# Kernel optimization log

Hardware: AMD Instinct MI355X
Metric: run time of the kernel (lower is better)

Reference implementation:

```python
import jax, jax.numpy as jnp
import numpy as np

B, S, D = 1, 2048, 2048
N_HEAD, N_KV = 32, 8
HD = D // N_HEAD  # 64


def make_freqs_cis(seq_len, head_dim, base=10000.0):
    inv = 1.0 / (base ** (np.arange(0, head_dim, 2, dtype=np.float32) / head_dim))
    t = np.arange(seq_len, dtype=np.float32)
    f = np.outer(t, inv)  # [S, HD/2]
    return jnp.asarray(np.stack([np.cos(f), np.sin(f)], axis=-1))  # [S, HD/2, 2]


def setup_inputs() -> dict:
    key = jax.random.key(0)
    k1, k2, k3 = jax.random.split(key, 3)
    scale = 1.0 / np.sqrt(D)
    return {
        "hidden_states": jax.random.normal(k1, (B, S, D), jnp.float32),
        "freqs_cis": make_freqs_cis(S, HD),
        "wqkv": jax.random.normal(k2, ((N_HEAD + 2 * N_KV) * HD, D), jnp.float32) * scale,
        "wo": jax.random.normal(k3, (D, D), jnp.float32) * scale,
    }


def apply_rotary(x, freqs_cis):
    # x: [B, S, H, HD]; freqs_cis: [S, HD/2, 2]
    xs = x.reshape(*x.shape[:-1], HD // 2, 2)
    cos = freqs_cis[None, :, None, :, 0]
    sin = freqs_cis[None, :, None, :, 1]
    x0, x1 = xs[..., 0], xs[..., 1]
    out = jnp.stack([x0 * cos - x1 * sin, x1 * cos + x0 * sin], axis=-1)
    return out.reshape(x.shape)


def reference(hidden_states, freqs_cis, wqkv, wo):
    bsz, seq_len, _ = hidden_states.shape
    kv_size = N_KV * HD
    qkv = hidden_states @ wqkv.T  # [B, S, 3072]
    q, k, v = jnp.split(qkv, [D, D + kv_size], axis=-1)
    q = q.reshape(bsz, seq_len, N_HEAD, HD)
    k = k.reshape(bsz, seq_len, N_KV, HD)
    v = v.reshape(bsz, seq_len, N_KV, HD)
    q = apply_rotary(q, freqs_cis)
    k = apply_rotary(k, freqs_cis)
    # [B, H, S, HD]
    q = q.transpose(0, 2, 1, 3)
    k = k.transpose(0, 2, 1, 3)
    v = v.transpose(0, 2, 1, 3)
    rep = N_HEAD // N_KV
    k = jnp.repeat(k, rep, axis=1)
    v = jnp.repeat(v, rep, axis=1)
    scores = jnp.einsum("bhqd,bhkd->bhqk", q, k) / jnp.sqrt(jnp.float32(HD))
    causal = jnp.tril(jnp.ones((seq_len, seq_len), bool))
    scores = jnp.where(causal[None, None], scores, jnp.finfo(scores.dtype).min)
    attn = jax.nn.softmax(scores, axis=-1)
    out = jnp.einsum("bhqk,bhkd->bhqd", attn, v)
    out = out.transpose(0, 2, 1, 3).reshape(bsz, seq_len, D)
    return out @ wo.T
```

## Files before the change

### kernel.cpp

```cpp
#include <hip/hip_runtime.h>

typedef unsigned short u16;
typedef __attribute__((ext_vector_type(8))) short bf16x8;
typedef __attribute__((ext_vector_type(4))) float f32x4;

#define MFMA16(a, b, c) __builtin_amdgcn_mfma_f32_16x16x32_bf16((a), (b), (c), 0, 0, 0)
#define EXP2(x) __builtin_amdgcn_exp2f(x)

#define S 2048
#define D 2048
#define NH 32
#define NKV 8
#define HD 64
#define QKV_N 3072

__device__ __forceinline__ u16 f2bf(float f) {
  unsigned int u = __float_as_uint(f);
  u += 0x7fffu + ((u >> 16) & 1u);
  return (u16)(u >> 16);
}

__device__ __forceinline__ void glds16(const void* g, void* l) {
  __builtin_amdgcn_global_load_lds((const __attribute__((address_space(1))) unsigned int*)g,
                                   (__attribute__((address_space(3))) unsigned int*)l,
                                   16, 0, 0);
}

#define N1 (S * D / 4)
#define N2 (QKV_N * D / 4)
#define N3 (D * D / 4)
__global__ void cast_all(const float* __restrict__ hs, const float* __restrict__ wqkv,
                         const float* __restrict__ wo, u16* __restrict__ o1,
                         u16* __restrict__ o2, u16* __restrict__ o3) {
  int i = blockIdx.x * blockDim.x + threadIdx.x;
  const float* src;
  u16* dst;
  int idx;
  if (i < N1) { src = hs; dst = o1; idx = i; }
  else if (i < N1 + N2) { src = wqkv; dst = o2; idx = i - N1; }
  else if (i < N1 + N2 + N3) { src = wo; dst = o3; idx = i - N1 - N2; }
  else return;
  float4 v = ((const float4*)src)[idx];
  ushort4 o;
  o.x = f2bf(v.x); o.y = f2bf(v.y); o.z = f2bf(v.z); o.w = f2bf(v.w);
  ((ushort4*)dst)[idx] = o;
}

#define GEMM_MAINLOOP(A_, B_, K_, bm_, bn_)                                            \
  const int srowS = lane >> 3, scolS = ((lane & 7) ^ srowS) * 8;                       \
  const int aBase = wave * 32, bBase = wave * 16;                                      \
  const int qq = lane >> 4, sw = lr & 7;                                               \
  _Pragma("unroll") for (int c2 = 0; c2 < 4; ++c2)                                     \
      glds16(A_ + (size_t)(bm_ + aBase + c2 * 8 + srowS) * K_ + scolS,                 \
             &sA[0][aBase + c2 * 8][0]);                                               \
  _Pragma("unroll") for (int c2 = 0; c2 < 2; ++c2)                                     \
      glds16(B_ + (size_t)(bn_ + bBase + c2 * 8 + srowS) * K_ + scolS,                 \
             &sB[0][bBase + c2 * 8][0]);                                               \
  const int nk = K_ >> 6;                                                              \
  for (int it = 0; it < nk; ++it) {                                                    \
    const int buf = it & 1;                                                            \
    __syncthreads();                                                                   \
    if (it + 1 < nk) {                                                                 \
      const int k1 = (it + 1) << 6;                                                    \
      _Pragma("unroll") for (int c2 = 0; c2 < 4; ++c2)                                 \
          glds16(A_ + (size_t)(bm_ + aBase + c2 * 8 + srowS) * K_ + k1 + scolS,        \
                 &sA[buf ^ 1][aBase + c2 * 8][0]);                                     \
      _Pragma("unroll") for (int c2 = 0; c2 < 2; ++c2)                                 \
          glds16(B_ + (size_t)(bn_ + bBase + c2 * 8 + srowS) * K_ + k1 + scolS,        \
                 &sB[buf ^ 1][bBase + c2 * 8][0]);                                     \
    }                                                                                  \
    bf16x8 af[2][2], bfr[2][4];                                                        \
    _Pragma("unroll") for (int c = 0; c < 2; ++c) {                                    \
      const int pc = (((c << 2) | qq) ^ sw) * 8;     \
      _Pragma("unroll") for (int i = 0; i < 2; ++i)                                    \
          af[c][i] = *(const bf16x8*)(&sA[buf][wr + i * 16 + lr][pc]);                 \
      _Pragma("unroll") for (int j = 0; j < 4; ++j)                                    \
          bfr[c][j] = *(const bf16x8*)(&sB[buf][j * 16 + lr][pc]);                     \
    }                                                                                  \
    _Pragma("unroll") for (int c = 0; c < 2; ++c)                                      \
        _Pragma("unroll") for (int i = 0; i < 2; ++i)                                  \
            _Pragma("unroll") for (int j = 0; j < 4; ++j)                              \
                acc[i][j] = MFMA16(af[c][i], bfr[c][j], acc[i][j]);                    \
  }

__global__ __launch_bounds__(256) void gemm_bt(const u16* __restrict__ A, const u16* __restrict__ B,
                                               float* __restrict__ C, int M, int N, int K) {
  __shared__ u16 sA[2][128][64];
  __shared__ u16 sB[2][64][64];
  const int tid = threadIdx.x;
  const int wave = tid >> 6, lane = tid & 63;
  const int bm = blockIdx.y * 128, bn = blockIdx.x * 64;
  const int lr = lane & 15, lk = (lane >> 4) * 8;
  const int wr = wave * 32;
  (void)lk;

  f32x4 acc[2][4] = {};
  GEMM_MAINLOOP(A, B, K, bm, bn)

  const int crb = (lane >> 4) * 4;
#pragma unroll
  for (int i = 0; i < 2; ++i)
#pragma unroll
    for (int j = 0; j < 4; ++j)
#pragma unroll
      for (int r = 0; r < 4; ++r) {
        int row = bm + wr + i * 16 + crb + r;
        int col = bn + j * 16 + lr;
        C[(size_t)row * N + col] = acc[i][j][r];
      }
}

#define QSCALE 0.18033688011112042f
__global__ __launch_bounds__(256) void gemm1_fused(const u16* __restrict__ A, const u16* __restrict__ B,
                                                   const float* __restrict__ fc,
                                                   u16* __restrict__ qo, u16* __restrict__ ko,
                                                   u16* __restrict__ vt) {
  __shared__ u16 sA[2][128][64];
  __shared__ u16 sB[2][64][64];
  const int tid = threadIdx.x;
  const int wave = tid >> 6, lane = tid & 63;
  const int bm = blockIdx.y * 128, bn = blockIdx.x * 64;
  const int lr = lane & 15, lk = (lane >> 4) * 8;
  const int wr = wave * 32;
  (void)lk;

  f32x4 acc[2][4] = {};
  GEMM_MAINLOOP(A, B, D, bm, bn)

  const int crb = (lane >> 4) * 4;

  if (bn < 2560) {
    const bool isQ = (bn < 2048);
    u16* dst_base = isQ ? (qo + (size_t)(bn >> 6) * S * HD)
                        : (ko + (size_t)((bn - 2048) >> 6) * S * HD);
    const float scale = isQ ? QSCALE : 1.0f;
    const int odd = lr & 1;
#pragma unroll
    for (int i = 0; i < 2; ++i)
#pragma unroll
      for (int r = 0; r < 4; ++r) {
        const int srow = bm + wr + i * 16 + crb + r;
#pragma unroll
        for (int j = 0; j < 4; ++j) {
          const int d = j * 16 + lr;
          float x = acc[i][j][r];
          float xp = __shfl_xor(x, 1, 64);
          float2 cs = *(const float2*)(fc + (size_t)srow * 64 + (d >> 1) * 2);
          float y = odd ? (x * cs.x + xp * cs.y) : (x * cs.x - xp * cs.y);
          dst_base[(size_t)srow * HD + d] = f2bf(y * scale);
        }
      }
  } else {
    const int kvh = (bn - 2560) >> 6;
    __syncthreads();
    u16(*sT)[136] = (u16(*)[136]) & sA[0][0][0];
#pragma unroll
    for (int i = 0; i < 2; ++i)
#pragma unroll
      for (int j = 0; j < 4; ++j)
#pragma unroll
        for (int r = 0; r < 4; ++r)
          sT[j * 16 + lr][wr + i * 16 + crb + r] = f2bf(acc[i][j][r]);
    __syncthreads();
    const int d = tid >> 2, sc = (tid & 3) * 32;
    uint4* dst = (uint4*)(vt + (size_t)kvh * HD * S + (size_t)d * S + bm + sc);
    const uint4* src = (const uint4*)(&sT[d][sc]);
    dst[0] = src[0];
    dst[1] = src[1];
    dst[2] = src[2];
    dst[3] = src[3];
  }
}

__global__ __launch_bounds__(256, 2) void attn_kernel(const u16* __restrict__ Q, const u16* __restrict__ Kc,
                                                      const u16* __restrict__ Vt, u16* __restrict__ Out) {
  __shared__ u16 sK[64][72];
  __shared__ u16 sV[64][72];
  __shared__ u16 sP[4][2][16][72];

  const int p = blockIdx.x;
  const int h = blockIdx.y;
  const int kvh = h >> 2;
  const int tid = threadIdx.x;
  const int wave = tid >> 6, lane = tid & 63;
  const int lr = lane & 15;
  const int lk = (lane >> 4) * 8;
  const int crb = (lane >> 4) * 4;
  const int t = 4 * p + wave;
  const int qbA = 16 * t;
  const int qbB = 16 * (127 - t);

  const u16* qpA = Q + ((size_t)h * S + qbA + lr) * HD;
  const u16* qpB = Q + ((size_t)h * S + qbB + lr) * HD;
  bf16x8 aA0 = *(const bf16x8*)(qpA + lk);
  bf16x8 aA1 = *(const bf16x8*)(qpA + 32 + lk);
  bf16x8 aB0 = *(const bf16x8*)(qpB + lk);
  bf16x8 aB1 = *(const bf16x8*)(qpB + 32 + lk);

  const u16* Kh = Kc + (size_t)kvh * S * HD;
  const u16* Vh = Vt + (size_t)kvh * HD * S;

  const int sr0 = tid >> 3, so0 = (tid & 7) * 8;
  const int sr1 = sr0 + 32;

  float lA[4] = {0.f, 0.f, 0.f, 0.f}, lB[4] = {0.f, 0.f, 0.f, 0.f};
  f32x4 oA[4] = {}, oB[4] = {};

  const int kend = (32 - p) * 64;

  uint4 pk0 = *(const uint4*)(Kh + (size_t)sr0 * HD + so0);
  uint4 pk1 = *(const uint4*)(Kh + (size_t)sr1 * HD + so0);
  uint4 pv0 = *(const uint4*)(Vh + (size_t)sr0 * S + so0);
  uint4 pv1 = *(const uint4*)(Vh + (size_t)sr1 * S + so0);

  bf16x8 vf[4][2];
  bf16x8 pfB[2], pfA[2];
  bool prevA = false;

  for (int kb = 0; kb < kend; kb += 64) {
    if (kb > 0) {
#pragma unroll
      for (int tt = 0; tt < 4; ++tt) {
        oB[tt] = MFMA16(pfB[0], vf[tt][0], oB[tt]);
        oB[tt] = MFMA16(pfB[1], vf[tt][1], oB[tt]);
      }
      if (prevA) {
#pragma unroll
        for (int tt = 0; tt < 4; ++tt) {
          oA[tt] = MFMA16(pfA[0], vf[tt][0], oA[tt]);
          oA[tt] = MFMA16(pfA[1], vf[tt][1], oA[tt]);
        }
      }
    }

    *(uint4*)(&sK[sr0][so0]) = pk0;
    *(uint4*)(&sK[sr1][so0]) = pk1;
    *(uint4*)(&sV[sr0][so0]) = pv0;
    *(uint4*)(&sV[sr1][so0]) = pv1;
    __syncthreads();

    const int kn = kb + 64;
    if (kn < kend) {
      pk0 = *(const uint4*)(Kh + (size_t)(kn + sr0) * HD + so0);
      pk1 = *(const uint4*)(Kh + (size_t)(kn + sr1) * HD + so0);
      pv0 = *(const uint4*)(Vh + (size_t)sr0 * S + kn + so0);
      pv1 = *(const uint4*)(Vh + (size_t)sr1 * S + kn + so0);
    }

    const bool liveA = (kb <= qbA + 15);

    f32x4 cA[4], cB[4];
#pragma unroll
    for (int tt = 0; tt < 4; ++tt) {
      bf16x8 b0 = *(const bf16x8*)(&sK[tt * 16 + lr][lk]);
      bf16x8 b1 = *(const bf16x8*)(&sK[tt * 16 + lr][32 + lk]);
      f32x4 zB = {};
      zB = MFMA16(aB0, b0, zB);
      cB[tt] = MFMA16(aB1, b1, zB);
      if (liveA) {
        f32x4 zA = {};
        zA = MFMA16(aA0, b0, zA);
        cA[tt] = MFMA16(aA1, b1, zA);
      }
    }

    if (kb + 63 <= qbB) {
#pragma unroll
      for (int r = 0; r < 4; ++r)
#pragma unroll
        for (int tt = 0; tt < 4; ++tt) {
          float pp = EXP2(cB[tt][r] - 8.0f);
          lB[r] += pp;
          sP[wave][0][crb + r][tt * 16 + lr] = f2bf(pp);
        }
    } else {
#pragma unroll
      for (int r = 0; r < 4; ++r) {
        const int qr = qbB + crb + r;
#pragma unroll
        for (int tt = 0; tt < 4; ++tt) {
          float pp = (kb + tt * 16 + lr <= qr) ? EXP2(cB[tt][r] - 8.0f) : 0.0f;
          lB[r] += pp;
          sP[wave][0][crb + r][tt * 16 + lr] = f2bf(pp);
        }
      }
    }

    if (liveA) {
      if (kb + 63 <= qbA) {
#pragma unroll
        for (int r = 0; r < 4; ++r)
#pragma unroll
          for (int tt = 0; tt < 4; ++tt) {
            float pp = EXP2(cA[tt][r] - 8.0f);
            lA[r] += pp;
            sP[wave][1][crb + r][tt * 16 + lr] = f2bf(pp);
          }
      } else {
#pragma unroll
        for (int r = 0; r < 4; ++r) {
          const int qr = qbA + crb + r;
#pragma unroll
          for (int tt = 0; tt < 4; ++tt) {
            float pp = (kb + tt * 16 + lr <= qr) ? EXP2(cA[tt][r] - 8.0f) : 0.0f;
            lA[r] += pp;
            sP[wave][1][crb + r][tt * 16 + lr] = f2bf(pp);
          }
        }
      }
    }

    pfB[0] = *(const bf16x8*)(&sP[wave][0][lr][lk]);
    pfB[1] = *(const bf16x8*)(&sP[wave][0][lr][32 + lk]);
    if (liveA) {
      pfA[0] = *(const bf16x8*)(&sP[wave][1][lr][lk]);
      pfA[1] = *(const bf16x8*)(&sP[wave][1][lr][32 + lk]);
    }
#pragma unroll
    for (int tt = 0; tt < 4; ++tt) {
      vf[tt][0] = *(const bf16x8*)(&sV[tt * 16 + lr][lk]);
      vf[tt][1] = *(const bf16x8*)(&sV[tt * 16 + lr][32 + lk]);
    }
    prevA = liveA;
    __syncthreads();
  }

#pragma unroll
  for (int tt = 0; tt < 4; ++tt) {
    oB[tt] = MFMA16(pfB[0], vf[tt][0], oB[tt]);
    oB[tt] = MFMA16(pfB[1], vf[tt][1], oB[tt]);
  }
  if (prevA) {
#pragma unroll
    for (int tt = 0; tt < 4; ++tt) {
      oA[tt] = MFMA16(pfA[0], vf[tt][0], oA[tt]);
      oA[tt] = MFMA16(pfA[1], vf[tt][1], oA[tt]);
    }
  }

#pragma unroll
  for (int r = 0; r < 4; ++r) {
#pragma unroll
    for (int off = 1; off < 16; off <<= 1) {
      lA[r] += __shfl_xor(lA[r], off, 64);
      lB[r] += __shfl_xor(lB[r], off, 64);
    }
    lA[r] = 1.0f / lA[r];
    lB[r] = 1.0f / lB[r];
  }
#pragma unroll
  for (int tt = 0; tt < 4; ++tt)
#pragma unroll
    for (int r = 0; r < 4; ++r) {
      const int d = tt * 16 + lr;
      Out[(size_t)(qbA + crb + r) * D + h * HD + d] = f2bf(oA[tt][r] * lA[r]);
      Out[(size_t)(qbB + crb + r) * D + h * HD + d] = f2bf(oB[tt][r] * lB[r]);
    }
}

extern "C" void kernel_launch(void* const* d_in, const int* in_sizes, int n_in,
                              void* d_out, int out_size, void* d_ws, size_t ws_size,
                              hipStream_t stream) {
  const float* hs = (const float*)d_in[0];
  const float* fc = (const float*)d_in[1];
  const float* wqkv = (const float*)d_in[2];
  const float* wo = (const float*)d_in[3];
  float* out = (float*)d_out;
  char* ws = (char*)d_ws;

  u16* hs_bf   = (u16*)(ws);
  u16* wqkv_bf = (u16*)(ws + ((size_t)8 << 20));
  u16* wo_bf   = (u16*)(ws + ((size_t)20 << 20));
  u16* q_bf    = (u16*)(ws + ((size_t)28 << 20));
  u16* k_bf    = (u16*)(ws + ((size_t)36 << 20));
  u16* vt_bf   = (u16*)(ws + ((size_t)38 << 20));
  u16* attn_bf = (u16*)(ws + ((size_t)40 << 20));

  cast_all<<<(N1 + N2 + N3 + 255) / 256, 256, 0, stream>>>(hs, wqkv, wo, hs_bf, wqkv_bf, wo_bf);

  gemm1_fused<<<dim3(QKV_N / 64, S / 128), 256, 0, stream>>>(hs_bf, wqkv_bf, fc, q_bf, k_bf, vt_bf);

  attn_kernel<<<dim3(16, NH), 256, 0, stream>>>(q_bf, k_bf, vt_bf, attn_bf);

  gemm_bt<<<dim3(D / 64, S / 128), 256, 0, stream>>>(attn_bf, wo_bf, out, S, D, D);
}
```

Measured before the change: 204.6 us.

## Keep attention probabilities in registers via transposed QK and permlane packing

Swaps the QK^T MFMA operand order so each lane holds the score rows in the layout the PV MFMA needs as its A operand. Probabilities are then packed to bf16 with v_cvt_pk_bf16_f32 and redistributed with permlane32/16 swaps, so the per-wave LDS buffer and its store/load round trip go away. The row-sum bookkeeping becomes one scalar per lane, reduced at the end with cross-group shuffles. The risk is the exact lane mapping of the permlane shuffles, which must be right for the output to be correct.

```diff
diff --git a/kernel.cpp b/kernel.cpp
--- a/kernel.cpp
+++ b/kernel.cpp
@@ -24,6 +24,29 @@
   __builtin_amdgcn_global_load_lds((const __attribute__((address_space(1))) unsigned int*)g,
                                    (__attribute__((address_space(3))) unsigned int*)l,
                                    16, 0, 0);
+}
+
+__device__ __forceinline__ unsigned int cvtpk(float lo, float hi) {
+  unsigned int r;
+  asm("v_cvt_pk_bf16_f32 %0, %1, %2" : "=v"(r) : "v"(lo), "v"(hi));
+  return r;
+}
+__device__ __forceinline__ void swap32(unsigned int& a, unsigned int& b) {
+  asm("v_permlane32_swap_b32 %0, %1" : "+v"(a), "+v"(b));
+}
+__device__ __forceinline__ void swap16(unsigned int& a, unsigned int& b) {
+  asm("v_permlane16_swap_b32 %0, %1" : "+v"(a), "+v"(b));
+}
+__device__ __forceinline__ bf16x8 pack4(const f32x4 c0, const f32x4 c1) {
+  unsigned int x0 = cvtpk(c0[0], c0[1]);
+  unsigned int x1 = cvtpk(c0[2], c0[3]);
+  unsigned int y0 = cvtpk(c1[0], c1[1]);
+  unsigned int y1 = cvtpk(c1[2], c1[3]);
+  swap32(x0, y0); swap16(x0, y0);
+  swap32(x1, y1); swap16(x1, y1);
+  union { bf16x8 v; unsigned int u[4]; } r;
+  r.u[0] = x0; r.u[1] = x1; r.u[2] = y0; r.u[3] = y1;
+  return r.v;
 }
 
 #define N1 (S * D / 4)
@@ -176,7 +199,6 @@
                                                       const u16* __restrict__ Vt, u16* __restrict__ Out) {
   __shared__ u16 sK[64][72];
   __shared__ u16 sV[64][72];
-  __shared__ u16 sP[4][2][16][72];
 
   const int p = blockIdx.x;
   const int h = blockIdx.y;
@@ -203,7 +225,7 @@
   const int sr0 = tid >> 3, so0 = (tid & 7) * 8;
   const int sr1 = sr0 + 32;
 
-  float lA[4] = {0.f, 0.f, 0.f, 0.f}, lB[4] = {0.f, 0.f, 0.f, 0.f};
+  float lA = 0.f, lB = 0.f;
   f32x4 oA[4] = {}, oB[4] = {};
 
   const int kend = (32 - p) * 64;
@@ -255,72 +277,74 @@
       bf16x8 b0 = *(const bf16x8*)(&sK[tt * 16 + lr][lk]);
       bf16x8 b1 = *(const bf16x8*)(&sK[tt * 16 + lr][32 + lk]);
       f32x4 zB = {};
-      zB = MFMA16(aB0, b0, zB);
-      cB[tt] = MFMA16(aB1, b1, zB);
+      zB = MFMA16(b0, aB0, zB);
+      cB[tt] = MFMA16(b1, aB1, zB);
       if (liveA) {
         f32x4 zA = {};
-        zA = MFMA16(aA0, b0, zA);
-        cA[tt] = MFMA16(aA1, b1, zA);
-      }
-    }
-
-    if (kb + 63 <= qbB) {
-#pragma unroll
-      for (int r = 0; r < 4; ++r)
-#pragma unroll
-        for (int tt = 0; tt < 4; ++tt) {
-          float pp = EXP2(cB[tt][r] - 8.0f);
-          lB[r] += pp;
-          sP[wave][0][crb + r][tt * 16 + lr] = f2bf(pp);
-        }
-    } else {
-#pragma unroll
-      for (int r = 0; r < 4; ++r) {
-        const int qr = qbB + crb + r;
-#pragma unroll
-        for (int tt = 0; tt < 4; ++tt) {
-          float pp = (kb + tt * 16 + lr <= qr) ? EXP2(cB[tt][r] - 8.0f) : 0.0f;
-          lB[r] += pp;
-          sP[wave][0][crb + r][tt * 16 + lr] = f2bf(pp);
-        }
-      }
-    }
-
-    if (liveA) {
-      if (kb + 63 <= qbA) {
-#pragma unroll
-        for (int r = 0; r < 4; ++r)
-#pragma unroll
-          for (int tt = 0; tt < 4; ++tt) {
-            float pp = EXP2(cA[tt][r] - 8.0f);
-            lA[r] += pp;
-            sP[wave][1][crb + r][tt * 16 + lr] = f2bf(pp);
-          }
-      } else {
-#pragma unroll
-        for (int r = 0; r < 4; ++r) {
-          const int qr = qbA + crb + r;
-#pragma unroll
-          for (int tt = 0; tt < 4; ++tt) {
-            float pp = (kb + tt * 16 + lr <= qr) ? EXP2(cA[tt][r] - 8.0f) : 0.0f;
-            lA[r] += pp;
-            sP[wave][1][crb + r][tt * 16 + lr] = f2bf(pp);
-          }
-        }
-      }
-    }
-
-    pfB[0] = *(const bf16x8*)(&sP[wave][0][lr][lk]);
-    pfB[1] = *(const bf16x8*)(&sP[wave][0][lr][32 + lk]);
-    if (liveA) {
-      pfA[0] = *(const bf16x8*)(&sP[wave][1][lr][lk]);
-      pfA[1] = *(const bf16x8*)(&sP[wave][1][lr][32 + lk]);
-    }
+        zA = MFMA16(b0, aA0, zA);
+        cA[tt] = MFMA16(b1, aA1, zA);
+      }
+    }
+
 #pragma unroll
     for (int tt = 0; tt < 4; ++tt) {
       vf[tt][0] = *(const bf16x8*)(&sV[tt * 16 + lr][lk]);
       vf[tt][1] = *(const bf16x8*)(&sV[tt * 16 + lr][32 + lk]);
     }
+
+    {
+      f32x4 pB[4];
+      if (kb + 63 <= qbB) {
+#pragma unroll
+        for (int tt = 0; tt < 4; ++tt)
+#pragma unroll
+          for (int r = 0; r < 4; ++r) {
+            float pp = EXP2(cB[tt][r] - 8.0f);
+            lB += pp;
+            pB[tt][r] = pp;
+          }
+      } else {
+        const int q = qbB + lr;
+#pragma unroll
+        for (int tt = 0; tt < 4; ++tt)
+#pragma unroll
+          for (int r = 0; r < 4; ++r) {
+            const int k = kb + tt * 16 + crb + r;
+            float pp = (k <= q) ? EXP2(cB[tt][r] - 8.0f) : 0.0f;
+            lB += pp;
+            pB[tt][r] = pp;
+          }
+      }
+      pfB[0] = pack4(pB[0], pB[1]);
+      pfB[1] = pack4(pB[2], pB[3]);
+    }
+
+    if (liveA) {
+      f32x4 pA[4];
+      if (kb + 63 <= qbA) {
+#pragma unroll
+        for (int tt = 0; tt < 4; ++tt)
+#pragma unroll
+          for (int r = 0; r < 4; ++r) {
+            float pp = EXP2(cA[tt][r] - 8.0f);
+            lA += pp;
+            pA[tt][r] = pp;
+          }
+      } else {
+        const int q = qbA + lr;
+#pragma unroll
+        for (int tt = 0; tt < 4; ++tt)
+#pragma unroll
+          for (int r = 0; r < 4; ++r) {
+            const int k = kb + tt * 16 + crb + r;
+            float pp = (k <= q) ? EXP2(cA[tt][r] - 8.0f) : 0.0f;
+            lA += pp;
+            pA[tt][r] = pp;
+          }
+      }
+      pfA[0] = pack4(pA[0], pA[1]);
+      pfA[1] = pack4(pA[2], pA[3]);
+    }
     prevA = liveA;
     __syncthreads();
   }
@@ -338,23 +362,23 @@
     }
   }
 
+  lA += __shfl_xor(lA, 16, 64);
+  lA += __shfl_xor(lA, 32, 64);
+  lB += __shfl_xor(lB, 16, 64);
+  lB += __shfl_xor(lB, 32, 64);
+  float rA[4], rB[4];
 #pragma unroll
   for (int r = 0; r < 4; ++r) {
-#pragma unroll
-    for (int off = 1; off < 16; off <<= 1) {
-      lA[r] += __shfl_xor(lA[r], off, 64);
-      lB[r] += __shfl_xor(lB[r], off, 64);
-    }
-    lA[r] = 1.0f / lA[r];
-    lB[r] = 1.0f / lB[r];
+    rA[r] = 1.0f / __shfl(lA, crb + r, 64);
+    rB[r] = 1.0f / __shfl(lB, crb + r, 64);
   }
 #pragma unroll
   for (int tt = 0; tt < 4; ++tt)
 #pragma unroll
     for (int r = 0; r < 4; ++r) {
       const int d = tt * 16 + lr;
-      Out[(size_t)(qbA + crb + r) * D + h * HD + d] = f2bf(oA[tt][r] * lA[r]);
-      Out[(size_t)(qbB + crb + r) * D + h * HD + d] = f2bf(oB[tt][r] * lB[r]);
+      Out[(size_t)(qbA + crb + r) * D + h * HD + d] = f2bf(oA[tt][r] * rA[r]);
+      Out[(size_t)(qbB + crb + r) * D + h * HD + d] = f2bf(oB[tt][r] * rB[r]);
     }
 }
 
```

Result: faster. 197.2 us (-3.7%).
